# Kernel tuning notes

Measured on AMD Instinct MI355X. Metric: run time of the kernel, lower is better.

The kernel has to match this reference:

```python
import jax, jax.numpy as jnp
import numpy as np

INPUT_DIM, HIDDEN_DIM, OUTPUT_DIM = 13, 256, 80


def setup_inputs() -> dict:
    key = jax.random.key(0)
    ks = jax.random.split(key, 5)
    x = jax.random.normal(ks[0], (64, 2048, INPUT_DIM), dtype=jnp.float32)
    # Xavier-uniform init like init_weights(); biases zero.
    def xavier(k, fan_in, fan_out):
        lim = np.sqrt(6.0 / (fan_in + fan_out)).astype(np.float32)
        return jax.random.uniform(k, (fan_in, fan_out), jnp.float32, -lim, lim)
    W1 = xavier(ks[1], INPUT_DIM, HIDDEN_DIM)
    W2 = xavier(ks[2], HIDDEN_DIM, HIDDEN_DIM)
    W3 = xavier(ks[3], HIDDEN_DIM, HIDDEN_DIM)
    W4 = xavier(ks[4], HIDDEN_DIM, OUTPUT_DIM)
    b1 = jnp.zeros((HIDDEN_DIM,), jnp.float32)
    b2 = jnp.zeros((HIDDEN_DIM,), jnp.float32)
    b3 = jnp.zeros((HIDDEN_DIM,), jnp.float32)
    b4 = jnp.zeros((OUTPUT_DIM,), jnp.float32)
    return {"x": x, "W1": W1, "b1": b1, "W2": W2, "b2": b2,
            "W3": W3, "b3": b3, "W4": W4, "b4": b4}


def reference(x, W1, b1, W2, b2, W3, b3, W4, b4):
    # Original loops over timesteps, but each timestep is an identical
    # Linear+ReLU stack -> collapse batch*seq into one batched matmul chain.
    h = jax.nn.relu(jnp.einsum('bsi,ih->bsh', x, W1) + b1)   # encoder L1
    h = jax.nn.relu(jnp.einsum('bsh,hk->bsk', h, W2) + b2)   # encoder L2
    h = jax.nn.relu(jnp.einsum('bsh,hk->bsk', h, W3) + b3)   # decoder L1
    out = jnp.einsum('bsh,ho->bso', h, W4) + b4              # decoder L2 (no ReLU)
    return out
```

## Files before the change

### kernel.cpp

```cpp
#include <hip/hip_runtime.h>


typedef _Float16 half_t;
typedef _Float16 half8 __attribute__((ext_vector_type(8)));
typedef float f32x16 __attribute__((ext_vector_type(16)));
typedef unsigned int uint4v __attribute__((ext_vector_type(4)));
typedef int int2v __attribute__((ext_vector_type(2)));

#define M_TOTAL (64*2048)

__global__ void prep_w(const float* __restrict__ W1, const float* __restrict__ W2,
                       const float* __restrict__ W3, const float* __restrict__ W4,
                       half_t* __restrict__ wp) {
    int tid = blockIdx.x * 256 + threadIdx.x;
    if (tid >= 312 * 512) return;
    int blk = tid >> 9, r = tid & 511;
    int lane = r >> 3, j = r & 7;
    const float* W; int K, N, nt, ks;
    if (blk < 8)        { W = W1; K = 13;  N = 256; nt = blk;              ks = 0; }
    else if (blk < 136) { W = W2; K = 256; N = 256; nt = (blk-8) >> 4;     ks = (blk-8) & 15; }
    else if (blk < 264) { W = W3; K = 256; N = 256; nt = (blk-136) >> 4;   ks = (blk-136) & 15; }
    else                { W = W4; K = 256; N = 80;  nt = (blk-264) >> 4;   ks = (blk-264) & 15; }
    int k = ks * 16 + (lane >> 5) * 8 + j;
    int n = nt * 32 + (lane & 31);
    float v = (k < K && n < N) ? W[k * N + n] : 0.f;
    wp[tid] = (half_t)v;
}


__device__ __forceinline__ unsigned int pkrtz(float a, float b) {
    auto p = __builtin_amdgcn_cvt_pkrtz(a, b);
    return __builtin_bit_cast(unsigned int, p);
}

typedef const __attribute__((address_space(1))) unsigned int guint_t;
typedef __attribute__((address_space(3))) unsigned int luint_t;

__device__ __forceinline__ void stage_strip(const half_t* __restrict__ g,
                                            half_t* l, int bytes, int tid) {
    const char* gc = (const char*)g;
    char* lc = (char*)l;
    const int go = tid * 16;
    const int lo = (tid >> 6) << 10;
#pragma unroll
    for (int r = 0; r < bytes; r += 4096) {
        __builtin_amdgcn_global_load_lds((guint_t*)(gc + r + go),
                                         (luint_t*)(lc + r + lo), 16, 0, 0);
    }
}

__device__ __forceinline__ int strip_off(int s) {
    if (s == 0)  return 0;
    if (s <= 8)  return (8   + (s - 1)  * 16) * 512;
    if (s <= 16) return (136 + (s - 9)  * 16) * 512;
    return (264 + (s - 17) * 16) * 512;
}

#define PIPE_BAR(Nstr) do {                                   \
    asm volatile("s_waitcnt vmcnt(" Nstr ")" ::: "memory");   \
    __builtin_amdgcn_sched_barrier(0);                        \
    __builtin_amdgcn_s_barrier();                             \
    __builtin_amdgcn_sched_barrier(0);                        \
} while (0)

template <int NKS, bool RELU>
__device__ __forceinline__ void dense_tile(const half_t* astrip,
                                           const unsigned int (&Bin)[16][4],
                                           unsigned int (*Bout)[4],
                                           const float* biasnt, int lane, bool hi)
{
    f32x16 acc = {};
#pragma unroll
    for (int ks = 0; ks < NKS; ++ks) {
        half8 a = *(const half8*)(astrip + ((ks * 64 + lane) << 3));
        uint4v bw = { Bin[ks][0], Bin[ks][1], Bin[ks][2], Bin[ks][3] };
        acc = __builtin_amdgcn_mfma_f32_32x32x16_f16(a, __builtin_bit_cast(half8, bw),
                                                     acc, 0, 0, 0);
    }
#pragma unroll
    for (int s = 0; s < 2; ++s) {
        float v[8];
#pragma unroll
        for (int q = 0; q < 8; ++q) {
            int f = (q & 3) + 8 * (q >> 2) + (hi ? 4 : 0);
            float t = acc[8 * s + q] + biasnt[16 * s + f];
            v[q] = RELU ? fmaxf(t, 0.f) : t;
        }
        unsigned int P0 = pkrtz(v[0], v[1]);
        unsigned int P1 = pkrtz(v[2], v[3]);
        unsigned int P2 = pkrtz(v[4], v[5]);
        unsigned int P3 = pkrtz(v[6], v[7]);
        int2v r02 = __builtin_amdgcn_permlane32_swap((int)P0, (int)P2, false, false);
        int2v r13 = __builtin_amdgcn_permlane32_swap((int)P1, (int)P3, false, false);
        Bout[s][0] = (unsigned int)r02.x;
        Bout[s][1] = (unsigned int)r13.x;
        Bout[s][2] = (unsigned int)r02.y;
        Bout[s][3] = (unsigned int)r13.y;
    }
}

__device__ __forceinline__ void out_tile(const half_t* astrip,
                                         const unsigned int (&Bin)[16][4],
                                         const float* biasnt, float* __restrict__ out,
                                         int m0, int nt, int lane, bool hi)
{
    f32x16 acc = {};
#pragma unroll
    for (int ks = 0; ks < 16; ++ks) {
        half8 a = *(const half8*)(astrip + ((ks * 64 + lane) << 3));
        uint4v bw = { Bin[ks][0], Bin[ks][1], Bin[ks][2], Bin[ks][3] };
        acc = __builtin_amdgcn_mfma_f32_32x32x16_f16(a, __builtin_bit_cast(half8, bw),
                                                     acc, 0, 0, 0);
    }
    float* orow = out + (long)(m0 + (lane & 31)) * 80 + nt * 32;
#pragma unroll
    for (int reg = 0; reg < 16; ++reg) {
        if (nt == 2 && (reg >> 2) >= 2) continue;
        int rr = (reg & 3) + 8 * (reg >> 2) + (hi ? 4 : 0);
        orow[rr] = acc[reg] + biasnt[rr];
    }
}

__global__ __launch_bounds__(256, 2) void mlp_mfma(
    const float* __restrict__ x, const half_t* __restrict__ wp,
    const float* __restrict__ b1, const float* __restrict__ b2,
    const float* __restrict__ b3, const float* __restrict__ b4,
    float* __restrict__ out)
{
    __shared__ half_t wbuf[3][8192];
    __shared__ float  bias_lds[864];

    const int tid  = threadIdx.x;
    const int lane = tid & 63;
    const bool hi  = lane >= 32;
    const int m0   = (blockIdx.x * 4 + (tid >> 6)) * 32;

    bias_lds[tid] = b1[tid];
    bias_lds[256 + tid] = b2[tid];
    bias_lds[512 + tid] = b3[tid];
    if (tid < 96) bias_lds[768 + tid] = (tid < 80) ? b4[tid] : 0.f;

    stage_strip(wp + strip_off(0), wbuf[0], 8192, tid);
    stage_strip(wp + strip_off(1), wbuf[1], 16384, tid);

    unsigned int BA[16][4], BB[16][4];

    {
        const float* xp = x + (long)(m0 + (lane & 31)) * 13;
        float xv[8];
        if (!hi) {
#pragma unroll
            for (int j = 0; j < 8; ++j) xv[j] = xp[j];
        } else {
#pragma unroll
            for (int j = 0; j < 5; ++j) xv[j] = xp[8 + j];
            xv[5] = xv[6] = xv[7] = 0.f;
        }
        BA[0][0] = pkrtz(xv[0], xv[1]);
        BA[0][1] = pkrtz(xv[2], xv[3]);
        BA[0][2] = pkrtz(xv[4], xv[5]);
        BA[0][3] = pkrtz(xv[6], xv[7]);
    }

    __syncthreads();

    stage_strip(wp + strip_off(2), wbuf[2], 16384, tid);
#pragma unroll
    for (int nt = 0; nt < 8; ++nt)
        dense_tile<1, true>(&wbuf[0][nt * 512], BA, &BB[2 * nt],
                            bias_lds + nt * 32, lane, hi);

#pragma unroll
    for (int i = 0; i < 8; ++i) {
        const int k = 1 + i;
        PIPE_BAR("4");
        stage_strip(wp + strip_off(k + 2), wbuf[(k + 2) % 3], 16384, tid);
        dense_tile<16, true>(&wbuf[k % 3][0], BB, &BA[2 * i],
                             bias_lds + 256 + i * 32, lane, hi);
    }

#pragma unroll
    for (int i = 0; i < 8; ++i) {
        const int k = 9 + i;
        PIPE_BAR("4");
        stage_strip(wp + strip_off(k + 2), wbuf[(k + 2) % 3], 16384, tid);
        dense_tile<16, true>(&wbuf[k % 3][0], BA, &BB[2 * i],
                             bias_lds + 512 + i * 32, lane, hi);
    }

#pragma unroll
    for (int i = 0; i < 3; ++i) {
        const int k = 17 + i;
        if (i < 2) PIPE_BAR("4");
        else       PIPE_BAR("0");
        if (i == 0) stage_strip(wp + strip_off(19), wbuf[19 % 3], 16384, tid);
        out_tile(&wbuf[k % 3][0], BB, bias_lds + 768 + i * 32, out, m0, i, lane, hi);
    }
}


extern "C" void kernel_launch(void* const* d_in, const int* in_sizes, int n_in,
                              void* d_out, int out_size, void* d_ws, size_t ws_size,
                              hipStream_t stream) {
    const float* x  = (const float*)d_in[0];
    const float* W1 = (const float*)d_in[1];
    const float* b1 = (const float*)d_in[2];
    const float* W2 = (const float*)d_in[3];
    const float* b2 = (const float*)d_in[4];
    const float* W3 = (const float*)d_in[5];
    const float* b3 = (const float*)d_in[6];
    const float* W4 = (const float*)d_in[7];
    const float* b4 = (const float*)d_in[8];
    float* out = (float*)d_out;

    half_t* wp = (half_t*)d_ws;

    hipLaunchKernelGGL(prep_w, dim3(624), dim3(256), 0, stream, W1, W2, W3, W4, wp);
    hipLaunchKernelGGL(mlp_mfma, dim3(M_TOTAL / 128), dim3(256), 0, stream,
                       x, wp, b1, b2, b3, b4, out);
}
```

Baseline: 53.73 us.

## Process 64 rows per wave to reuse each weight fragment across two MFMAs

Each wave now handles two 32-row groups instead of one. Every LDS weight fragment it reads feeds two MFMA accumulators, and the grid shrinks by half. This halves the LDS weight reads and the global weight staging per output row. In exchange the register-resident activation buffers double to about 256 dwords per lane under the same launch bounds, so register spills or lower occupancy become likely.

```diff
diff --git a/kernel.cpp b/kernel.cpp
--- a/kernel.cpp
+++ b/kernel.cpp
@@ -63,61 +63,81 @@
     __builtin_amdgcn_sched_barrier(0);                        \
 } while (0)
 
+template <bool RELU>
+__device__ __forceinline__ void repack(const f32x16& acc, int s,
+                                       const float* biasnt, bool hi,
+                                       unsigned int* Bw)
+{
+    float v[8];
+#pragma unroll
+    for (int q = 0; q < 8; ++q) {
+        int f = (q & 3) + 8 * (q >> 2) + (hi ? 4 : 0);
+        float t = acc[8 * s + q] + biasnt[16 * s + f];
+        v[q] = RELU ? fmaxf(t, 0.f) : t;
+    }
+    unsigned int P0 = pkrtz(v[0], v[1]);
+    unsigned int P1 = pkrtz(v[2], v[3]);
+    unsigned int P2 = pkrtz(v[4], v[5]);
+    unsigned int P3 = pkrtz(v[6], v[7]);
+    int2v r02 = __builtin_amdgcn_permlane32_swap((int)P0, (int)P2, false, false);
+    int2v r13 = __builtin_amdgcn_permlane32_swap((int)P1, (int)P3, false, false);
+    Bw[0] = (unsigned int)r02.x;
+    Bw[1] = (unsigned int)r13.x;
+    Bw[2] = (unsigned int)r02.y;
+    Bw[3] = (unsigned int)r13.y;
+}
+
 template <int NKS, bool RELU>
-__device__ __forceinline__ void dense_tile(const half_t* astrip,
-                                           const unsigned int (&Bin)[16][4],
-                                           unsigned int (*Bout)[4],
-                                           const float* biasnt, int lane, bool hi)
-{
-    f32x16 acc = {};
+__device__ __forceinline__ void dense_tile2(const half_t* astrip,
+                                            const unsigned int (&Bin)[2][16][4],
+                                            unsigned int (*Bout0)[4],
+                                            unsigned int (*Bout1)[4],
+                                            const float* biasnt, int lane, bool hi)
+{
+    f32x16 acc0 = {}, acc1 = {};
 #pragma unroll
     for (int ks = 0; ks < NKS; ++ks) {
         half8 a = *(const half8*)(astrip + ((ks * 64 + lane) << 3));
-        uint4v bw = { Bin[ks][0], Bin[ks][1], Bin[ks][2], Bin[ks][3] };
-        acc = __builtin_amdgcn_mfma_f32_32x32x16_f16(a, __builtin_bit_cast(half8, bw),
-                                                     acc, 0, 0, 0);
+        uint4v b0 = { Bin[0][ks][0], Bin[0][ks][1], Bin[0][ks][2], Bin[0][ks][3] };
+        uint4v b1 = { Bin[1][ks][0], Bin[1][ks][1], Bin[1][ks][2], Bin[1][ks][3] };
+        acc0 = __builtin_amdgcn_mfma_f32_32x32x16_f16(a, __builtin_bit_cast(half8, b0),
+                                                      acc0, 0, 0, 0);
+        acc1 = __builtin_amdgcn_mfma_f32_32x32x16_f16(a, __builtin_bit_cast(half8, b1),
+                                                      acc1, 0, 0, 0);
     }
 #pragma unroll
     for (int s = 0; s < 2; ++s) {
-        float v[8];
-#pragma unroll
-        for (int q = 0; q < 8; ++q) {
-            int f = (q & 3) + 8 * (q >> 2) + (hi ? 4 : 0);
-            float t = acc[8 * s + q] + biasnt[16 * s + f];
-            v[q] = RELU ? fmaxf(t, 0.f) : t;
-        }
-        unsigned int P0 = pkrtz(v[0], v[1]);
-        unsigned int P1 = pkrtz(v[2], v[3]);
-        unsigned int P2 = pkrtz(v[4], v[5]);
-        unsigned int P3 = pkrtz(v[6], v[7]);
-        int2v r02 = __builtin_amdgcn_permlane32_swap((int)P0, (int)P2, false, false);
-        int2v r13 = __builtin_amdgcn_permlane32_swap((int)P1, (int)P3, false, false);
-        Bout[s][0] = (unsigned int)r02.x;
-        Bout[s][1] = (unsigned int)r13.x;
-        Bout[s][2] = (unsigned int)r02.y;
-        Bout[s][3] = (unsigned int)r13.y;
-    }
-}
-
-__device__ __forceinline__ void out_tile(const half_t* astrip,
-                                         const unsigned int (&Bin)[16][4],
-                                         const float* biasnt, float* __restrict__ out,
-                                         int m0, int nt, int lane, bool hi)
-{
-    f32x16 acc = {};
+        repack<RELU>(acc0, s, biasnt, hi, Bout0[s]);
+        repack<RELU>(acc1, s, biasnt, hi, Bout1[s]);
+    }
+}
+
+__device__ __forceinline__ void out_tile2(const half_t* astrip,
+                                          const unsigned int (&Bin)[2][16][4],
+                                          const float* biasnt, float* __restrict__ out,
+                                          int m0, int nt, int lane, bool hi)
+{
+    f32x16 acc0 = {}, acc1 = {};
 #pragma unroll
     for (int ks = 0; ks < 16; ++ks) {
         half8 a = *(const half8*)(astrip + ((ks * 64 + lane) << 3));
-        uint4v bw = { Bin[ks][0], Bin[ks][1], Bin[ks][2], Bin[ks][3] };
-        acc = __builtin_amdgcn_mfma_f32_32x32x16_f16(a, __builtin_bit_cast(half8, bw),
-                                                     acc, 0, 0, 0);
-    }
-    float* orow = out + (long)(m0 + (lane & 31)) * 80 + nt * 32;
-#pragma unroll
-    for (int reg = 0; reg < 16; ++reg) {
-        if (nt == 2 && (reg >> 2) >= 2) continue;
-        int rr = (reg & 3) + 8 * (reg >> 2) + (hi ? 4 : 0);
-        orow[rr] = acc[reg] + biasnt[rr];
+        uint4v b0 = { Bin[0][ks][0], Bin[0][ks][1], Bin[0][ks][2], Bin[0][ks][3] };
+        uint4v b1 = { Bin[1][ks][0], Bin[1][ks][1], Bin[1][ks][2], Bin[1][ks][3] };
+        acc0 = __builtin_amdgcn_mfma_f32_32x32x16_f16(a, __builtin_bit_cast(half8, b0),
+                                                      acc0, 0, 0, 0);
+        acc1 = __builtin_amdgcn_mfma_f32_32x32x16_f16(a, __builtin_bit_cast(half8, b1),
+                                                      acc1, 0, 0, 0);
+    }
+#pragma unroll
+    for (int g = 0; g < 2; ++g) {
+        const f32x16& acc = g ? acc1 : acc0;
+        float* orow = out + (long)(m0 + g * 32 + (lane & 31)) * 80 + nt * 32;
+#pragma unroll
+        for (int reg = 0; reg < 16; ++reg) {
+            if (nt == 2 && (reg >> 2) >= 2) continue;
+            int rr = (reg & 3) + 8 * (reg >> 2) + (hi ? 4 : 0);
+            orow[rr] = acc[reg] + biasnt[rr];
+        }
     }
 }
 
@@ -133,7 +153,7 @@
     const int tid  = threadIdx.x;
     const int lane = tid & 63;
     const bool hi  = lane >= 32;
-    const int m0   = (blockIdx.x * 4 + (tid >> 6)) * 32;
+    const int m0   = (blockIdx.x * 4 + (tid >> 6)) * 64;
 
     bias_lds[tid] = b1[tid];
     bias_lds[256 + tid] = b2[tid];
@@ -143,10 +163,11 @@
     stage_strip(wp + strip_off(0), wbuf[0], 8192, tid);
     stage_strip(wp + strip_off(1), wbuf[1], 16384, tid);
 
-    unsigned int BA[16][4], BB[16][4];
-
-    {
-        const float* xp = x + (long)(m0 + (lane & 31)) * 13;
+    unsigned int BA[2][16][4], BB[2][16][4];
+
+#pragma unroll
+    for (int g = 0; g < 2; ++g) {
+        const float* xp = x + (long)(m0 + g * 32 + (lane & 31)) * 13;
         float xv[8];
         if (!hi) {
 #pragma unroll
@@ -156,10 +177,10 @@
             for (int j = 0; j < 5; ++j) xv[j] = xp[8 + j];
             xv[5] = xv[6] = xv[7] = 0.f;
         }
-        BA[0][0] = pkrtz(xv[0], xv[1]);
-        BA[0][1] = pkrtz(xv[2], xv[3]);
-        BA[0][2] = pkrtz(xv[4], xv[5]);
-        BA[0][3] = pkrtz(xv[6], xv[7]);
+        BA[g][0][0] = pkrtz(xv[0], xv[1]);
+        BA[g][0][1] = pkrtz(xv[2], xv[3]);
+        BA[g][0][2] = pkrtz(xv[4], xv[5]);
+        BA[g][0][3] = pkrtz(xv[6], xv[7]);
     }
 
     __syncthreads();
@@ -167,16 +188,16 @@
     stage_strip(wp + strip_off(2), wbuf[2], 16384, tid);
 #pragma unroll
     for (int nt = 0; nt < 8; ++nt)
-        dense_tile<1, true>(&wbuf[0][nt * 512], BA, &BB[2 * nt],
-                            bias_lds + nt * 32, lane, hi);
+        dense_tile2<1, true>(&wbuf[0][nt * 512], BA, &BB[0][2 * nt], &BB[1][2 * nt],
+                             bias_lds + nt * 32, lane, hi);
 
 #pragma unroll
     for (int i = 0; i < 8; ++i) {
         const int k = 1 + i;
         PIPE_BAR("4");
         stage_strip(wp + strip_off(k + 2), wbuf[(k + 2) % 3], 16384, tid);
-        dense_tile<16, true>(&wbuf[k % 3][0], BB, &BA[2 * i],
-                             bias_lds + 256 + i * 32, lane, hi);
+        dense_tile2<16, true>(&wbuf[k % 3][0], BB, &BA[0][2 * i], &BA[1][2 * i],
+                              bias_lds + 256 + i * 32, lane, hi);
     }
 
 #pragma unroll
@@ -184,8 +205,8 @@
         const int k = 9 + i;
         PIPE_BAR("4");
         stage_strip(wp + strip_off(k + 2), wbuf[(k + 2) % 3], 16384, tid);
-        dense_tile<16, true>(&wbuf[k % 3][0], BA, &BB[2 * i],
-                             bias_lds + 512 + i * 32, lane, hi);
+        dense_tile2<16, true>(&wbuf[k % 3][0], BA, &BB[0][2 * i], &BB[1][2 * i],
+                              bias_lds + 512 + i * 32, lane, hi);
     }
 
 #pragma unroll
@@ -194,7 +215,7 @@
         if (i < 2) PIPE_BAR("4");
         else       PIPE_BAR("0");
         if (i == 0) stage_strip(wp + strip_off(19), wbuf[19 % 3], 16384, tid);
-        out_tile(&wbuf[k % 3][0], BB, bias_lds + 768 + i * 32, out, m0, i, lane, hi);
+        out_tile2(&wbuf[k % 3][0], BB, bias_lds + 768 + i * 32, out, m0, i, lane, hi);
     }
 }
 
@@ -216,6 +237,6 @@
     half_t* wp = (half_t*)d_ws;
 
     hipLaunchKernelGGL(prep_w, dim3(624), dim3(256), 0, stream, W1, W2, W3, W4, wp);
-    hipLaunchKernelGGL(mlp_mfma, dim3(M_TOTAL / 128), dim3(256), 0, stream,
+    hipLaunchKernelGGL(mlp_mfma, dim3(M_TOTAL / 256), dim3(256), 0, stream,
                        x, wp, b1, b2, b3, b4, out);
 }
```

New measurement: 56.01 us. 4.2% more time.

## Switch weight staging to double-buffered 32KB strips with fewer barriers and MFMA priority

Applied to the files above, without the earlier changes.

Replaces the triple-buffered 16KB weight-strip pipeline, which used explicit vmcnt waits and a barrier per 32-column tile, with a double-buffered scheme. Each stage now loads a 32KB strip covering two output tiles. This roughly halves the number of barrier points in the layer chain. It also raises wave priority around the MFMA loops with s_setprio. The trade-off is shallower prefetch: each __syncthreads now waits for the next strip's loads to finish, so only one stage of compute hides each load.

```diff
diff --git a/kernel.cpp b/kernel.cpp
--- a/kernel.cpp
+++ b/kernel.cpp
@@ -51,17 +51,14 @@
 
 __device__ __forceinline__ int strip_off(int s) {
     if (s == 0)  return 0;
-    if (s <= 8)  return (8   + (s - 1)  * 16) * 512;
-    if (s <= 16) return (136 + (s - 9)  * 16) * 512;
-    return (264 + (s - 17) * 16) * 512;
-}
-
-#define PIPE_BAR(Nstr) do {                                   \
-    asm volatile("s_waitcnt vmcnt(" Nstr ")" ::: "memory");   \
-    __builtin_amdgcn_sched_barrier(0);                        \
-    __builtin_amdgcn_s_barrier();                             \
-    __builtin_amdgcn_sched_barrier(0);                        \
-} while (0)
+    if (s <= 4)  return (8   + (s - 1) * 32) * 512;
+    if (s <= 8)  return (136 + (s - 5) * 32) * 512;
+    if (s == 9)  return 264 * 512;
+    return 296 * 512;
+}
+__device__ __forceinline__ int strip_bytes(int s) {
+    return (s == 0) ? 8192 : (s == 10 ? 16384 : 32768);
+}
 
 template <int NKS, bool RELU>
 __device__ __forceinline__ void dense_tile(const half_t* astrip,
@@ -70,6 +67,7 @@
                                            const float* biasnt, int lane, bool hi)
 {
     f32x16 acc = {};
+    __builtin_amdgcn_s_setprio(1);
 #pragma unroll
     for (int ks = 0; ks < NKS; ++ks) {
         half8 a = *(const half8*)(astrip + ((ks * 64 + lane) << 3));
@@ -77,6 +75,7 @@
         acc = __builtin_amdgcn_mfma_f32_32x32x16_f16(a, __builtin_bit_cast(half8, bw),
                                                      acc, 0, 0, 0);
     }
+    __builtin_amdgcn_s_setprio(0);
 #pragma unroll
     for (int s = 0; s < 2; ++s) {
         float v[8];
@@ -105,6 +104,7 @@
                                          int m0, int nt, int lane, bool hi)
 {
     f32x16 acc = {};
+    __builtin_amdgcn_s_setprio(1);
 #pragma unroll
     for (int ks = 0; ks < 16; ++ks) {
         half8 a = *(const half8*)(astrip + ((ks * 64 + lane) << 3));
@@ -112,6 +112,7 @@
         acc = __builtin_amdgcn_mfma_f32_32x32x16_f16(a, __builtin_bit_cast(half8, bw),
                                                      acc, 0, 0, 0);
     }
+    __builtin_amdgcn_s_setprio(0);
     float* orow = out + (long)(m0 + (lane & 31)) * 80 + nt * 32;
 #pragma unroll
     for (int reg = 0; reg < 16; ++reg) {
@@ -127,7 +128,7 @@
     const float* __restrict__ b3, const float* __restrict__ b4,
     float* __restrict__ out)
 {
-    __shared__ half_t wbuf[3][8192];
+    __shared__ half_t wbuf[2][16384];
     __shared__ float  bias_lds[864];
 
     const int tid  = threadIdx.x;
@@ -135,14 +136,13 @@
     const bool hi  = lane >= 32;
     const int m0   = (blockIdx.x * 4 + (tid >> 6)) * 32;
 
+    stage_strip(wp + strip_off(0), wbuf[0], 8192, tid);
+
     bias_lds[tid] = b1[tid];
     bias_lds[256 + tid] = b2[tid];
     bias_lds[512 + tid] = b3[tid];
     if (tid < 96) bias_lds[768 + tid] = (tid < 80) ? b4[tid] : 0.f;
 
-    stage_strip(wp + strip_off(0), wbuf[0], 8192, tid);
-    stage_strip(wp + strip_off(1), wbuf[1], 16384, tid);
-
     unsigned int BA[16][4], BB[16][4];
 
     {
@@ -164,38 +164,53 @@
 
     __syncthreads();
 
-    stage_strip(wp + strip_off(2), wbuf[2], 16384, tid);
+    stage_strip(wp + strip_off(1), wbuf[1], 32768, tid);
+    __builtin_amdgcn_sched_barrier(0);
 #pragma unroll
     for (int nt = 0; nt < 8; ++nt)
         dense_tile<1, true>(&wbuf[0][nt * 512], BA, &BB[2 * nt],
                             bias_lds + nt * 32, lane, hi);
-
-#pragma unroll
-    for (int i = 0; i < 8; ++i) {
-        const int k = 1 + i;
-        PIPE_BAR("4");
-        stage_strip(wp + strip_off(k + 2), wbuf[(k + 2) % 3], 16384, tid);
-        dense_tile<16, true>(&wbuf[k % 3][0], BB, &BA[2 * i],
-                             bias_lds + 256 + i * 32, lane, hi);
-    }
-
-#pragma unroll
-    for (int i = 0; i < 8; ++i) {
-        const int k = 9 + i;
-        PIPE_BAR("4");
-        stage_strip(wp + strip_off(k + 2), wbuf[(k + 2) % 3], 16384, tid);
-        dense_tile<16, true>(&wbuf[k % 3][0], BA, &BB[2 * i],
-                             bias_lds + 512 + i * 32, lane, hi);
-    }
-
-#pragma unroll
-    for (int i = 0; i < 3; ++i) {
-        const int k = 17 + i;
-        if (i < 2) PIPE_BAR("4");
-        else       PIPE_BAR("0");
-        if (i == 0) stage_strip(wp + strip_off(19), wbuf[19 % 3], 16384, tid);
-        out_tile(&wbuf[k % 3][0], BB, bias_lds + 768 + i * 32, out, m0, i, lane, hi);
-    }
+    __syncthreads();
+
+#pragma unroll
+    for (int p = 1; p <= 4; ++p) {
+        if (p < 10) {
+            stage_strip(wp + strip_off(p + 1), wbuf[(p + 1) & 1], strip_bytes(p + 1), tid);
+            __builtin_amdgcn_sched_barrier(0);
+        }
+        const half_t* sb = &wbuf[p & 1][0];
+#pragma unroll
+        for (int sub = 0; sub < 2; ++sub) {
+            const int nt = (p - 1) * 2 + sub;
+            dense_tile<16, true>(sb + sub * 16 * 512, BB, &BA[2 * nt],
+                                 bias_lds + 256 + nt * 32, lane, hi);
+        }
+        __syncthreads();
+    }
+
+#pragma unroll
+    for (int p = 5; p <= 8; ++p) {
+        stage_strip(wp + strip_off(p + 1), wbuf[(p + 1) & 1], strip_bytes(p + 1), tid);
+        __builtin_amdgcn_sched_barrier(0);
+        const half_t* sb = &wbuf[p & 1][0];
+#pragma unroll
+        for (int sub = 0; sub < 2; ++sub) {
+            const int nt = (p - 5) * 2 + sub;
+            dense_tile<16, true>(sb + sub * 16 * 512, BA, &BB[2 * nt],
+                                 bias_lds + 512 + nt * 32, lane, hi);
+        }
+        __syncthreads();
+    }
+
+    stage_strip(wp + strip_off(10), wbuf[0], 16384, tid);
+    __builtin_amdgcn_sched_barrier(0);
+#pragma unroll
+    for (int sub = 0; sub < 2; ++sub)
+        out_tile(&wbuf[1][sub * 16 * 512], BB, bias_lds + 768 + sub * 32,
+                 out, m0, sub, lane, hi);
+    __syncthreads();
+
+    out_tile(&wbuf[0][0], BB, bias_lds + 768 + 64, out, m0, 2, lane, hi);
 }
 
 
```

Result: slower. 55.09 us (+2.5%).
